# Kernel tuning notes

Measured on AMD Instinct MI355X. Metric: run time of the kernel, lower is better.

## Reference

```python
import jax, jax.numpy as jnp
import numpy as np

DIM = 96
D_STATE = 16
D_CONV = 3
D_INNER = 192   # int(DIM * 2.0)
DT_RANK = 6     # ceil(DIM / 16)
K = 4           # cross-scan directions
BATCH, H, W = 2, 56, 56


def setup_inputs() -> dict:
    key = jax.random.key(0)
    k = jax.random.split(key, 8)
    x = jax.random.normal(k[0], (BATCH, DIM, H, W), jnp.float32)
    W_in = jax.random.normal(k[1], (DIM, 2 * D_INNER), jnp.float32) / np.sqrt(DIM)
    W_conv = jax.random.normal(k[2], (D_INNER, 1, D_CONV, D_CONV), jnp.float32) / D_CONV
    b_conv = jnp.zeros((D_INNER,), jnp.float32)
    W_xproj = jax.random.normal(k[3], (K, D_INNER, DT_RANK + 2 * D_STATE), jnp.float32) / np.sqrt(D_INNER)
    W_dt = jax.random.normal(k[4], (K, DT_RANK, D_INNER), jnp.float32) / np.sqrt(DT_RANK)
    # dt bias init as in torch: dt ~ exp(U * (log 0.1 - log 0.001) + log 0.001), inv-softplus
    dt = jnp.exp(jax.random.uniform(k[5], (K, D_INNER), jnp.float32)
                 * (np.log(0.1) - np.log(0.001)) + np.log(0.001))
    dt = jnp.clip(dt, 1e-4, None)
    b_dt = dt + jnp.log(-jnp.expm1(-dt))
    A_logs = jnp.log(jnp.broadcast_to(jnp.arange(1, D_STATE + 1, dtype=jnp.float32),
                                      (K, D_INNER, D_STATE)))
    Ds = jnp.ones((K, D_INNER), jnp.float32)
    W_out = jax.random.normal(k[6], (D_INNER, DIM), jnp.float32) / np.sqrt(D_INNER)
    return dict(x=x, W_in=W_in, W_conv=W_conv, b_conv=b_conv, W_xproj=W_xproj,
                W_dt=W_dt, b_dt=b_dt, A_logs=A_logs, Ds=Ds, W_out=W_out)


def _ss2d(x, W_in, W_conv, b_conv, W_xproj, W_dt, b_dt, A_logs, Ds, W_out):
    Bsz, C, Hh, Ww = x.shape
    L = Hh * Ww
    # in_proj
    xf = x.transpose(0, 2, 3, 1).reshape(Bsz, L, C)        # (B, L, C)
    xz = xf @ W_in
    xp, z = jnp.split(xz, 2, axis=-1)                       # each (B, L, D)
    # depthwise conv + silu
    xi = xp.reshape(Bsz, Hh, Ww, -1).transpose(0, 3, 1, 2)  # (B, D, H, W)
    pad = D_CONV // 2
    xi = jax.lax.conv_general_dilated(
        xi, W_conv, (1, 1), ((pad, pad), (pad, pad)),
        feature_group_count=xi.shape[1],
        dimension_numbers=('NCHW', 'OIHW', 'NCHW')) + b_conv[None, :, None, None]
    xi = jax.nn.silu(xi)
    D = xi.shape[1]
    # cross-scan: 4 directions, each (B, L, D)
    x1 = xi.reshape(Bsz, D, L).transpose(0, 2, 1)
    x2 = xi[:, :, :, ::-1].reshape(Bsz, D, L).transpose(0, 2, 1)
    xt = xi.transpose(0, 1, 3, 2)                           # (B, D, W, H)
    x3 = xt.reshape(Bsz, D, L).transpose(0, 2, 1)
    x4 = xt[:, :, :, ::-1].reshape(Bsz, D, L).transpose(0, 2, 1)
    xs = jnp.stack([x1, x2, x3, x4])                        # (K, B, L, D)
    # per-direction projections, batched over K
    xdbl = jnp.einsum('kbld,kde->kble', xs, W_xproj)
    dr = xdbl[..., :DT_RANK]
    Bk = xdbl[..., DT_RANK:DT_RANK + D_STATE]               # (K, B, L, N)
    Ck = xdbl[..., DT_RANK + D_STATE:]                      # (K, B, L, N)
    delta = jax.nn.softplus(jnp.einsum('kblr,krd->kbld', dr, W_dt)
                            + b_dt[:, None, None, :])       # (K, B, L, D)
    A = -jnp.exp(A_logs)                                    # (K, D, N)

    def step(h, inp):
        x_i, d_i, B_i, C_i = inp  # (K,B,D), (K,B,D), (K,B,N), (K,B,N)
        dA = jnp.exp(d_i[..., None] * A[:, None])           # (K, B, D, N)
        h = dA * h + (d_i * x_i)[..., None] * B_i[:, :, None, :]
        y = jnp.einsum('kbdn,kbn->kbd', h, C_i)
        return h, y

    h0 = jnp.zeros((K, Bsz, D, D_STATE), xs.dtype)
    seq = (xs.transpose(2, 0, 1, 3), delta.transpose(2, 0, 1, 3),
           Bk.transpose(2, 0, 1, 3), Ck.transpose(2, 0, 1, 3))
    _, ys = jax.lax.scan(step, h0, seq)                     # (L, K, B, D)
    ys = ys.transpose(1, 2, 0, 3) + xs * Ds[:, None, None, :]  # (K, B, L, D)
    # cross-merge back to row-major (h w) order
    y1 = ys[0]
    y2 = ys[1].reshape(Bsz, Hh, Ww, D)[:, :, ::-1, :].reshape(Bsz, L, D)
    y3 = ys[2].reshape(Bsz, Ww, Hh, D).transpose(0, 2, 1, 3).reshape(Bsz, L, D)
    y4 = ys[3].reshape(Bsz, Ww, Hh, D)[:, :, ::-1, :].transpose(0, 2, 1, 3).reshape(Bsz, L, D)
    y = (y1 + y2 + y3 + y4) * jax.nn.silu(z)
    out = (y @ W_out).reshape(Bsz, Hh, Ww, C).transpose(0, 3, 1, 2)
    return out


def reference(x, W_in, W_conv, b_conv, W_xproj, W_dt, b_dt, A_logs, Ds, W_out):
    return _ss2d(x, W_in, W_conv, b_conv, W_xproj, W_dt, b_dt, A_logs, Ds, W_out)
```

## Files before the change

### kernel.cpp

```cpp
#include <hip/hip_runtime.h>
#include <math.h>

constexpr int BATCH  = 2;
constexpr int CDIM   = 96;
constexpr int HH     = 56;
constexpr int WW     = 56;
constexpr int LL     = HH * WW;
constexpr int DIN    = 192;
constexpr int NK     = 4;
constexpr int NST    = 16;
constexpr int RNK    = 6;
constexpr int EPROJ  = RNK + 2 * NST;
constexpr int SCH    = 64;
constexpr int NCH    = LL / SCH;
constexpr int CGRP   = DIN / 16;

constexpr int STDU = SCH + 2;
constexpr int STBC = SCH + 6;
constexpr int STY  = SCH + 4;
constexpr int STB1 = SCH + 4;

constexpr size_t SZ_PX   = (size_t)BATCH * LL * DIN;
constexpr size_t OFF_XP  = 0;
constexpr size_t OFF_Z   = OFF_XP + SZ_PX;
constexpr size_t OFF_XI  = OFF_Z  + SZ_PX;
constexpr size_t OFF_DR  = OFF_XI + SZ_PX;
constexpr size_t SZ_DR   = (size_t)NK * BATCH * LL * 8;
constexpr size_t OFF_B   = OFF_DR + SZ_DR;
constexpr size_t SZ_BC   = (size_t)NK * BATCH * LL * NST;
constexpr size_t OFF_C   = OFF_B + SZ_BC;
constexpr size_t OFF_YD  = OFF_C + SZ_BC;
constexpr size_t SZ_YD   = (size_t)NK * BATCH * LL * DIN;
constexpr size_t OFF_HE  = OFF_YD + SZ_YD;
constexpr size_t SZ_HS   = (size_t)NK * BATCH * NCH * DIN * NST;
constexpr size_t OFF_HI  = OFF_HE + SZ_HS;
constexpr size_t OFF_WT  = OFF_HI + SZ_HS;
constexpr size_t SZ_WT   = (size_t)NK * EPROJ * DIN;

__device__ __forceinline__ float silu(float v) {
    return v / (1.0f + __expf(-v));
}

__device__ __forceinline__ float softplus_f(float x) {
    return (x > 20.0f) ? x : __logf(1.0f + __expf(x));
}

__device__ __forceinline__ float row_reduce16(float p) {
    p += __int_as_float(__builtin_amdgcn_update_dpp(0, __float_as_int(p), 0x128, 0xf, 0xf, true));
    p += __int_as_float(__builtin_amdgcn_update_dpp(0, __float_as_int(p), 0x124, 0xf, 0xf, true));
    p += __int_as_float(__builtin_amdgcn_update_dpp(0, __float_as_int(p), 0x122, 0xf, 0xf, true));
    p += __int_as_float(__builtin_amdgcn_update_dpp(0, __float_as_int(p), 0x121, 0xf, 0xf, true));
    return p;
}

__device__ __forceinline__ int seq_to_lr(int k, int l) {
    int q = l / WW;
    int r = l - q * WW;
    if (k == 0) return l;
    if (k == 1) return q * WW + (WW - 1 - r);
    if (k == 2) return r * WW + q;
    return (WW - 1 - r) * WW + q;
}

__device__ __forceinline__ int spatial_to_seq(int k, int s) {
    int h = s / WW;
    int w = s - h * WW;
    if (k == 0) return s;
    if (k == 1) return h * WW + (WW - 1 - w);
    if (k == 2) return w * WW + h;
    return w * WW + (WW - 1 - h);
}

__device__ __forceinline__ size_t hs_idx(int c, int kb, int d, int n) {
    return ((size_t)(c * (NK * BATCH) + kb) * DIN + d) * NST + n;
}

__device__ __forceinline__ float4 delta4(
        float4 r03, float2 r45, const float4* wr, float4 bb4) {
    float4 raw = bb4;
    raw.x = fmaf(r03.x, wr[0].x, raw.x); raw.y = fmaf(r03.x, wr[0].y, raw.y);
    raw.z = fmaf(r03.x, wr[0].z, raw.z); raw.w = fmaf(r03.x, wr[0].w, raw.w);
    raw.x = fmaf(r03.y, wr[1].x, raw.x); raw.y = fmaf(r03.y, wr[1].y, raw.y);
    raw.z = fmaf(r03.y, wr[1].z, raw.z); raw.w = fmaf(r03.y, wr[1].w, raw.w);
    raw.x = fmaf(r03.z, wr[2].x, raw.x); raw.y = fmaf(r03.z, wr[2].y, raw.y);
    raw.z = fmaf(r03.z, wr[2].z, raw.z); raw.w = fmaf(r03.z, wr[2].w, raw.w);
    raw.x = fmaf(r03.w, wr[3].x, raw.x); raw.y = fmaf(r03.w, wr[3].y, raw.y);
    raw.z = fmaf(r03.w, wr[3].z, raw.z); raw.w = fmaf(r03.w, wr[3].w, raw.w);
    raw.x = fmaf(r45.x, wr[4].x, raw.x); raw.y = fmaf(r45.x, wr[4].y, raw.y);
    raw.z = fmaf(r45.x, wr[4].z, raw.z); raw.w = fmaf(r45.x, wr[4].w, raw.w);
    raw.x = fmaf(r45.y, wr[5].x, raw.x); raw.y = fmaf(r45.y, wr[5].y, raw.y);
    raw.z = fmaf(r45.y, wr[5].z, raw.z); raw.w = fmaf(r45.y, wr[5].w, raw.w);
    raw.x = softplus_f(raw.x); raw.y = softplus_f(raw.y);
    raw.z = softplus_f(raw.z); raw.w = softplus_f(raw.w);
    return raw;
}

constexpr int K1_PIX = 8;
__global__ __launch_bounds__(384) void k_inproj(
        const float* __restrict__ x, const float* __restrict__ W_in,
        const float* __restrict__ W_xproj,
        float* __restrict__ xp, float* __restrict__ z, float* __restrict__ Wt) {
    __shared__ float sxT[CDIM][K1_PIX];
    int gp0 = blockIdx.x * K1_PIX;
    int t   = threadIdx.x;
    int b   = gp0 / LL;
    int l0  = gp0 - b * LL;
    int gid = blockIdx.x * 384 + t;
    if (gid < NK * DIN * EPROJ) {
        int k = gid / (DIN * EPROJ);
        int r = gid % (DIN * EPROJ);
        int d = r / EPROJ;
        int e = r % EPROJ;
        Wt[((size_t)k * EPROJ + e) * DIN + d] = W_xproj[gid];
    }
    for (int i = t; i < CDIM * K1_PIX; i += 384) {
        int c = i >> 3, p = i & 7;
        sxT[c][p] = x[((size_t)(b * CDIM + c)) * LL + l0 + p];
    }
    __syncthreads();
    int e = t;
    float acc[K1_PIX];
#pragma unroll
    for (int p = 0; p < K1_PIX; p++) acc[p] = 0.0f;
    const float4* sx4 = (const float4*)sxT;
#pragma unroll 4
    for (int c = 0; c < CDIM; c++) {
        float w  = W_in[c * (2 * DIN) + e];
        float4 va = sx4[2 * c];
        float4 vb = sx4[2 * c + 1];
        acc[0] = fmaf(va.x, w, acc[0]); acc[1] = fmaf(va.y, w, acc[1]);
        acc[2] = fmaf(va.z, w, acc[2]); acc[3] = fmaf(va.w, w, acc[3]);
        acc[4] = fmaf(vb.x, w, acc[4]); acc[5] = fmaf(vb.y, w, acc[5]);
        acc[6] = fmaf(vb.z, w, acc[6]); acc[7] = fmaf(vb.w, w, acc[7]);
    }
    if (e < DIN) {
#pragma unroll
        for (int p = 0; p < K1_PIX; p++)
            xp[((size_t)(gp0 + p)) * DIN + e] = acc[p];
    } else {
        int e2 = e - DIN;
#pragma unroll
        for (int p = 0; p < K1_PIX; p++)
            z[((size_t)(gp0 + p)) * DIN + e2] = acc[p];
    }
}

__global__ __launch_bounds__(192) void k_conv(
        const float* __restrict__ xp, const float* __restrict__ Wc,
        const float* __restrict__ bc, float* __restrict__ xi) {
    int gp = blockIdx.x;
    int d  = threadIdx.x;
    int b  = gp / LL;
    int l  = gp - b * LL;
    int h  = l / WW;
    int w  = l - h * WW;
    float acc = bc[d];
#pragma unroll
    for (int dy = -1; dy <= 1; dy++) {
        int hh = h + dy;
        if (hh < 0 || hh >= HH) continue;
#pragma unroll
        for (int dx = -1; dx <= 1; dx++) {
            int ww = w + dx;
            if (ww < 0 || ww >= WW) continue;
            acc = fmaf(xp[((size_t)b * LL + hh * WW + ww) * DIN + d],
                       Wc[d * 9 + (dy + 1) * 3 + (dx + 1)], acc);
        }
    }
    xi[(size_t)gp * DIN + d] = silu(acc);
}

constexpr int K3_PIX = 32;
__global__ __launch_bounds__(256) void k_xproj(
        const float* __restrict__ xi, const float* __restrict__ Wt,
        float* __restrict__ drbuf, float* __restrict__ Bbuf,
        float* __restrict__ Cbuf) {
    __shared__ float4 v4[K3_PIX][49];
    __shared__ float4 sw4[EPROJ][49];
    int k   = blockIdx.y;
    int gp0 = blockIdx.x * K3_PIX;
    int b   = gp0 / LL;
    int l0  = gp0 - b * LL;
    int t   = threadIdx.x;
    const float4* xin4 = (const float4*)(xi + (size_t)gp0 * DIN);
    for (int i = t; i < K3_PIX * 48; i += 256)
        v4[i / 48][i % 48] = xin4[i];
    const float4* wt4 = (const float4*)(Wt + (size_t)k * EPROJ * DIN);
    for (int i = t; i < EPROJ * 48; i += 256)
        sw4[i / 48][i % 48] = wt4[i];
    __syncthreads();
    int p0 = t & 15;
    int eg = t >> 4;
    bool has3 = (eg < EPROJ - 32);
    float acc[2][3] = {{0.f, 0.f, 0.f}, {0.f, 0.f, 0.f}};
    for (int j = 0; j < 48; j++) {
        float4 w0 = sw4[eg][j];
        float4 w1 = sw4[eg + 16][j];
        float4 w2 = has3 ? sw4[eg + 32][j] : make_float4(0.f, 0.f, 0.f, 0.f);
#pragma unroll
        for (int q = 0; q < 2; q++) {
            float4 vv = v4[p0 + 16 * q][j];
            acc[q][0] = fmaf(vv.x, w0.x, acc[q][0]); acc[q][0] = fmaf(vv.y, w0.y, acc[q][0]);
            acc[q][0] = fmaf(vv.z, w0.z, acc[q][0]); acc[q][0] = fmaf(vv.w, w0.w, acc[q][0]);
            acc[q][1] = fmaf(vv.x, w1.x, acc[q][1]); acc[q][1] = fmaf(vv.y, w1.y, acc[q][1]);
            acc[q][1] = fmaf(vv.z, w1.z, acc[q][1]); acc[q][1] = fmaf(vv.w, w1.w, acc[q][1]);
            acc[q][2] = fmaf(vv.x, w2.x, acc[q][2]); acc[q][2] = fmaf(vv.y, w2.y, acc[q][2]);
            acc[q][2] = fmaf(vv.z, w2.z, acc[q][2]); acc[q][2] = fmaf(vv.w, w2.w, acc[q][2]);
        }
    }
#pragma unroll
    for (int q = 0; q < 2; q++) {
        int p  = p0 + 16 * q;
        int ls = spatial_to_seq(k, l0 + p);
        size_t kb  = (size_t)(k * BATCH + b);
        size_t b8  = (kb * LL + ls) * 8;
        size_t b16 = (kb * LL + ls) * NST;
        if (eg < RNK) drbuf[b8 + eg] = acc[q][0];
        else          Bbuf[b16 + eg - RNK] = acc[q][0];
        int e1 = eg + 16;
        if (e1 < RNK + NST) Bbuf[b16 + e1 - RNK] = acc[q][1];
        else                Cbuf[b16 + e1 - RNK - NST] = acc[q][1];
        if (has3) Cbuf[b16 + eg + 32 - RNK - NST] = acc[q][2];
    }
}

__global__ __launch_bounds__(256) void k_scanA(
        const float* __restrict__ xi, const float* __restrict__ drbuf,
        const float* __restrict__ Bbuf, const float* __restrict__ A_logs,
        const float* __restrict__ W_dt, const float* __restrict__ b_dt,
        float* __restrict__ Pbuf, float* __restrict__ hend) {
    __shared__ float2 sDU2[16][STDU];
    __shared__ float  sB1t[16][STB1];
    int c   = blockIdx.x;
    int blk = blockIdx.y;
    int k   = blk / (BATCH * CGRP);
    int rem = blk % (BATCH * CGRP);
    int b   = rem / CGRP;
    int cg  = rem % CGRP;
    int d0  = cg * 16;
    int t    = threadIdx.x;
    int lane = t & 63, wave = t >> 6;
    int grp  = lane >> 4, n = lane & 15;
    int ch   = wave * 4 + grp;
    int d    = d0 + ch;
    float A = -__expf(A_logs[((size_t)(k * DIN + d)) * NST + n]);
    size_t kb = (size_t)(k * BATCH + b);
    const float* drp = drbuf + kb * LL * 8;
    const float* bp  = Bbuf  + kb * LL * NST;
    const float* up  = xi    + (size_t)b * LL * DIN;
    int ss  = t >> 2;
    int cc0 = (t & 3) * 4;
    float4 wr[RNK];
#pragma unroll
    for (int r = 0; r < RNK; r++)
        wr[r] = *(const float4*)(W_dt + ((size_t)k * RNK + r) * DIN + d0 + cc0);
    float4 bb4 = *(const float4*)(b_dt + k * DIN + d0 + cc0);
    int l0 = c * SCH;
    {
        int l  = l0 + ss;
        int lr = seq_to_lr(k, l);
        float4 r03 = *(const float4*)(drp + (size_t)l * 8);
        float2 r45 = *(const float2*)(drp + (size_t)l * 8 + 4);
        float4 dlt = delta4(r03, r45, wr, bb4);
        float4 u4  = *(const float4*)(up + (size_t)lr * DIN + d0 + cc0);
        float4 B4  = *(const float4*)(bp + (size_t)l * NST + cc0);
        sDU2[cc0 + 0][ss] = make_float2(dlt.x, dlt.x * u4.x);
        sDU2[cc0 + 1][ss] = make_float2(dlt.y, dlt.y * u4.y);
        sDU2[cc0 + 2][ss] = make_float2(dlt.z, dlt.z * u4.z);
        sDU2[cc0 + 3][ss] = make_float2(dlt.w, dlt.w * u4.w);
        sB1t[cc0 + 0][ss] = B4.x;
        sB1t[cc0 + 1][ss] = B4.y;
        sB1t[cc0 + 2][ss] = B4.z;
        sB1t[cc0 + 3][ss] = B4.w;
    }
    __syncthreads();
    float h = 0.0f, P = 1.0f;
#pragma unroll 2
    for (int s4 = 0; s4 < SCH; s4 += 4) {
        float4 duA = *(const float4*)&sDU2[ch][s4];
        float4 duB = *(const float4*)&sDU2[ch][s4 + 2];
        float4 bq  = *(const float4*)&sB1t[n][s4];
        float dA;
        dA = __expf(duA.x * A); h = fmaf(dA, h, duA.y * bq.x); P *= dA;
        dA = __expf(duA.z * A); h = fmaf(dA, h, duA.w * bq.y); P *= dA;
        dA = __expf(duB.x * A); h = fmaf(dA, h, duB.y * bq.z); P *= dA;
        dA = __expf(duB.z * A); h = fmaf(dA, h, duB.w * bq.w); P *= dA;
    }
    size_t idx = hs_idx(c, (int)kb, d, n);
    Pbuf[idx] = P;
    hend[idx] = h;
}

__global__ __launch_bounds__(256) void k_scanB(
        const float* __restrict__ Pbuf, const float* __restrict__ hend,
        float* __restrict__ hin) {
    int tid = blockIdx.x * 256 + threadIdx.x;
    int kb  = tid / (DIN * NST);
    int dn  = tid % (DIN * NST);
    float h = 0.0f;
    for (int c = 0; c < NCH; c++) {
        size_t idx = ((size_t)(c * (NK * BATCH) + kb)) * (DIN * NST) + dn;
        hin[idx] = h;
        h = fmaf(Pbuf[idx], h, hend[idx]);
    }
}

__global__ __launch_bounds__(256) void k_scanC(
        const float* __restrict__ xi, const float* __restrict__ drbuf,
        const float* __restrict__ Bbuf, const float* __restrict__ Cbuf,
        const float* __restrict__ A_logs, const float* __restrict__ W_dt,
        const float* __restrict__ b_dt, const float* __restrict__ hin,
        float* __restrict__ ydir) {
    __shared__ float2 sDU2[16][STDU];
    __shared__ float2 sBC2[16][STBC];
    __shared__ float  sY[16][STY];
    int c   = blockIdx.x;
    int blk = blockIdx.y;
    int k   = blk / (BATCH * CGRP);
    int rem = blk % (BATCH * CGRP);
    int b   = rem / CGRP;
    int cg  = rem % CGRP;
    int d0  = cg * 16;
    int t    = threadIdx.x;
    int lane = t & 63, wave = t >> 6;
    int grp  = lane >> 4, n = lane & 15;
    int ch   = wave * 4 + grp;
    int d    = d0 + ch;
    float A = -__expf(A_logs[((size_t)(k * DIN + d)) * NST + n]);
    size_t kb = (size_t)(k * BATCH + b);
    const float* drp = drbuf + kb * LL * 8;
    const float* bp  = Bbuf  + kb * LL * NST;
    const float* cp  = Cbuf  + kb * LL * NST;
    const float* up  = xi    + (size_t)b * LL * DIN;
    float*       yp  = ydir  + kb * LL * DIN;
    int ss  = t >> 2;
    int cc0 = (t & 3) * 4;
    float4 wr[RNK];
#pragma unroll
    for (int r = 0; r < RNK; r++)
        wr[r] = *(const float4*)(W_dt + ((size_t)k * RNK + r) * DIN + d0 + cc0);
    float4 bb4 = *(const float4*)(b_dt + k * DIN + d0 + cc0);
    int l0 = c * SCH;
    {
        int l  = l0 + ss;
        int lr = seq_to_lr(k, l);
        float4 r03 = *(const float4*)(drp + (size_t)l * 8);
        float2 r45 = *(const float2*)(drp + (size_t)l * 8 + 4);
        float4 dlt = delta4(r03, r45, wr, bb4);
        float4 u4  = *(const float4*)(up + (size_t)lr * DIN + d0 + cc0);
        float4 B4  = *(const float4*)(bp + (size_t)l * NST + cc0);
        float4 C4  = *(const float4*)(cp + (size_t)l * NST + cc0);
        sDU2[cc0 + 0][ss] = make_float2(dlt.x, dlt.x * u4.x);
        sDU2[cc0 + 1][ss] = make_float2(dlt.y, dlt.y * u4.y);
        sDU2[cc0 + 2][ss] = make_float2(dlt.z, dlt.z * u4.z);
        sDU2[cc0 + 3][ss] = make_float2(dlt.w, dlt.w * u4.w);
        sBC2[cc0 + 0][ss] = make_float2(B4.x, C4.x);
        sBC2[cc0 + 1][ss] = make_float2(B4.y, C4.y);
        sBC2[cc0 + 2][ss] = make_float2(B4.z, C4.z);
        sBC2[cc0 + 3][ss] = make_float2(B4.w, C4.w);
    }
    float h = hin[hs_idx(c, (int)kb, d, n)];
    __syncthreads();
#pragma unroll 2
    for (int s4 = 0; s4 < SCH; s4 += 4) {
        float4 duA = *(const float4*)&sDU2[ch][s4];
        float4 duB = *(const float4*)&sDU2[ch][s4 + 2];
        float4 bcA = *(const float4*)&sBC2[n][s4];
        float4 bcB = *(const float4*)&sBC2[n][s4 + 2];
        float dA, y0, y1, y2, y3;
        dA = __expf(duA.x * A); h = fmaf(dA, h, duA.y * bcA.x); y0 = row_reduce16(h * bcA.y);
        dA = __expf(duA.z * A); h = fmaf(dA, h, duA.w * bcA.z); y1 = row_reduce16(h * bcA.w);
        dA = __expf(duB.x * A); h = fmaf(dA, h, duB.y * bcB.x); y2 = row_reduce16(h * bcB.y);
        dA = __expf(duB.z * A); h = fmaf(dA, h, duB.w * bcB.z); y3 = row_reduce16(h * bcB.w);
        if (n == 0) *(float4*)&sY[ch][s4] = make_float4(y0, y1, y2, y3);
    }
    __syncthreads();
    for (int i = t; i < SCH * 16; i += 256) {
        int s = i >> 4, cc = i & 15;
        int lr = seq_to_lr(k, l0 + s);
        yp[(size_t)lr * DIN + d0 + cc] = sY[cc][s];
    }
}

constexpr int K5_PIX = 8;
__global__ __launch_bounds__(192) void k_out(
        const float* __restrict__ ydir, const float* __restrict__ xi,
        const float* __restrict__ zbuf, const float* __restrict__ Ds,
        const float* __restrict__ W_out, float* __restrict__ out) {
    __shared__ float g[DIN][12];
    __shared__ float so[CDIM][9];
    int gp0 = blockIdx.x * K5_PIX;
    int b   = gp0 / LL;
    int l0  = gp0 - b * LL;
    int t   = threadIdx.x;
    for (int i = t; i < K5_PIX * DIN; i += 192) {
        int p = i / DIN, dd = i % DIN;
        size_t off = (size_t)(gp0 + p) * DIN + dd;
        float y = ydir[off] + ydir[SZ_PX + off]
                + ydir[2 * SZ_PX + off] + ydir[3 * SZ_PX + off];
        float dsum = Ds[dd] + Ds[DIN + dd] + Ds[2 * DIN + dd] + Ds[3 * DIN + dd];
        y = fmaf(xi[off], dsum, y);
        g[dd][p] = y * silu(zbuf[off]);
    }
    __syncthreads();
    int f    = t % CDIM;
    int half = t / CDIM;
    float acc[4] = {0.f, 0.f, 0.f, 0.f};
#pragma unroll 4
    for (int dd = 0; dd < DIN; dd++) {
        float wv = W_out[dd * CDIM + f];
        float4 gv = *(const float4*)&g[dd][half * 4];
        acc[0] = fmaf(gv.x, wv, acc[0]);
        acc[1] = fmaf(gv.y, wv, acc[1]);
        acc[2] = fmaf(gv.z, wv, acc[2]);
        acc[3] = fmaf(gv.w, wv, acc[3]);
    }
#pragma unroll
    for (int p = 0; p < 4; p++) so[f][half * 4 + p] = acc[p];
    __syncthreads();
    for (int i = t; i < CDIM * K5_PIX; i += 192) {
        int f2 = i / K5_PIX, p2 = i % K5_PIX;
        out[((size_t)(b * CDIM + f2)) * LL + l0 + p2] = so[f2][p2];
    }
}

extern "C" void kernel_launch(void* const* d_in, const int* in_sizes, int n_in,
                              void* d_out, int out_size, void* d_ws, size_t ws_size,
                              hipStream_t stream) {
    const float* x       = (const float*)d_in[0];
    const float* W_in    = (const float*)d_in[1];
    const float* W_conv  = (const float*)d_in[2];
    const float* b_conv  = (const float*)d_in[3];
    const float* W_xproj = (const float*)d_in[4];
    const float* W_dt    = (const float*)d_in[5];
    const float* b_dt    = (const float*)d_in[6];
    const float* A_logs  = (const float*)d_in[7];
    const float* Ds      = (const float*)d_in[8];
    const float* W_out   = (const float*)d_in[9];
    float* out = (float*)d_out;
    float* ws  = (float*)d_ws;

    float* xp    = ws + OFF_XP;
    float* z     = ws + OFF_Z;
    float* xi    = ws + OFF_XI;
    float* drbuf = ws + OFF_DR;
    float* Bbuf  = ws + OFF_B;
    float* Cbuf  = ws + OFF_C;
    float* ydir  = ws + OFF_YD;
    float* hend  = ws + OFF_HE;
    float* hin   = ws + OFF_HI;
    float* Wt    = ws + OFF_WT;
    float* Pbuf  = xp;

    k_inproj<<<(BATCH * LL) / K1_PIX, 384, 0, stream>>>(x, W_in, W_xproj, xp, z, Wt);
    k_conv<<<BATCH * LL, DIN, 0, stream>>>(xp, W_conv, b_conv, xi);
    dim3 g3((BATCH * LL) / K3_PIX, NK);
    k_xproj<<<g3, 256, 0, stream>>>(xi, Wt, drbuf, Bbuf, Cbuf);
    dim3 gs(NCH, NK * BATCH * CGRP);
    k_scanA<<<gs, 256, 0, stream>>>(xi, drbuf, Bbuf, A_logs, W_dt, b_dt, Pbuf, hend);
    k_scanB<<<(NK * BATCH * DIN * NST) / 256, 256, 0, stream>>>(Pbuf, hend, hin);
    k_scanC<<<gs, 256, 0, stream>>>(xi, drbuf, Bbuf, Cbuf, A_logs, W_dt, b_dt, hin, ydir);
    k_out<<<(BATCH * LL) / K5_PIX, 192, 0, stream>>>(ydir, xi, z, Ds, W_out, out);
}
```

Baseline: 212.5 us.

## Fuse chunk-prefix scan into scanC and read xproj weights from global

Removes the separate k_scanB kernel. Each scanC block now recomputes its own incoming chunk state by walking Pbuf/hend over all earlier chunks, which drops one launch and the hin buffer. The cost is redundant serial work that grows with the chunk index, up to 48 dependent loads per thread for late chunks. Separately, k_xproj stops staging the projection weights in shared memory and reads them straight from global (cached) memory with an unroll of 4, cutting LDS use and a staging loop.

```diff
diff --git a/kernel.cpp b/kernel.cpp
--- a/kernel.cpp
+++ b/kernel.cpp
@@ -33,8 +33,7 @@
 constexpr size_t SZ_YD   = (size_t)NK * BATCH * LL * DIN;
 constexpr size_t OFF_HE  = OFF_YD + SZ_YD;
 constexpr size_t SZ_HS   = (size_t)NK * BATCH * NCH * DIN * NST;
-constexpr size_t OFF_HI  = OFF_HE + SZ_HS;
-constexpr size_t OFF_WT  = OFF_HI + SZ_HS;
+constexpr size_t OFF_WT  = OFF_HE + SZ_HS;
 constexpr size_t SZ_WT   = (size_t)NK * EPROJ * DIN;
 
 __device__ __forceinline__ float silu(float v) {
@@ -176,7 +175,6 @@
         float* __restrict__ drbuf, float* __restrict__ Bbuf,
         float* __restrict__ Cbuf) {
     __shared__ float4 v4[K3_PIX][49];
-    __shared__ float4 sw4[EPROJ][49];
     int k   = blockIdx.y;
     int gp0 = blockIdx.x * K3_PIX;
     int b   = gp0 / LL;
@@ -186,17 +184,16 @@
     for (int i = t; i < K3_PIX * 48; i += 256)
         v4[i / 48][i % 48] = xin4[i];
     const float4* wt4 = (const float4*)(Wt + (size_t)k * EPROJ * DIN);
-    for (int i = t; i < EPROJ * 48; i += 256)
-        sw4[i / 48][i % 48] = wt4[i];
     __syncthreads();
     int p0 = t & 15;
     int eg = t >> 4;
     bool has3 = (eg < EPROJ - 32);
     float acc[2][3] = {{0.f, 0.f, 0.f}, {0.f, 0.f, 0.f}};
+#pragma unroll 4
     for (int j = 0; j < 48; j++) {
-        float4 w0 = sw4[eg][j];
-        float4 w1 = sw4[eg + 16][j];
-        float4 w2 = has3 ? sw4[eg + 32][j] : make_float4(0.f, 0.f, 0.f, 0.f);
+        float4 w0 = wt4[eg * 48 + j];
+        float4 w1 = wt4[(eg + 16) * 48 + j];
+        float4 w2 = has3 ? wt4[(eg + 32) * 48 + j] : make_float4(0.f, 0.f, 0.f, 0.f);
 #pragma unroll
         for (int q = 0; q < 2; q++) {
             float4 vv = v4[p0 + 16 * q][j];
@@ -291,25 +288,12 @@
     hend[idx] = h;
 }
 
-__global__ __launch_bounds__(256) void k_scanB(
-        const float* __restrict__ Pbuf, const float* __restrict__ hend,
-        float* __restrict__ hin) {
-    int tid = blockIdx.x * 256 + threadIdx.x;
-    int kb  = tid / (DIN * NST);
-    int dn  = tid % (DIN * NST);
-    float h = 0.0f;
-    for (int c = 0; c < NCH; c++) {
-        size_t idx = ((size_t)(c * (NK * BATCH) + kb)) * (DIN * NST) + dn;
-        hin[idx] = h;
-        h = fmaf(Pbuf[idx], h, hend[idx]);
-    }
-}
-
 __global__ __launch_bounds__(256) void k_scanC(
         const float* __restrict__ xi, const float* __restrict__ drbuf,
         const float* __restrict__ Bbuf, const float* __restrict__ Cbuf,
         const float* __restrict__ A_logs, const float* __restrict__ W_dt,
-        const float* __restrict__ b_dt, const float* __restrict__ hin,
+        const float* __restrict__ b_dt,
+        const float* __restrict__ Pbuf, const float* __restrict__ hend,
         float* __restrict__ ydir) {
     __shared__ float2 sDU2[16][STDU];
     __shared__ float2 sBC2[16][STBC];
@@ -333,6 +317,11 @@
     const float* cp  = Cbuf  + kb * LL * NST;
     const float* up  = xi    + (size_t)b * LL * DIN;
     float*       yp  = ydir  + kb * LL * DIN;
+    float hin = 0.0f;
+    for (int j = 0; j < c; j++) {
+        size_t jx = hs_idx(j, (int)kb, d, n);
+        hin = fmaf(Pbuf[jx], hin, hend[jx]);
+    }
     int ss  = t >> 2;
     int cc0 = (t & 3) * 4;
     float4 wr[RNK];
@@ -359,8 +348,8 @@
         sBC2[cc0 + 2][ss] = make_float2(B4.z, C4.z);
         sBC2[cc0 + 3][ss] = make_float2(B4.w, C4.w);
     }
-    float h = hin[hs_idx(c, (int)kb, d, n)];
-    __syncthreads();
+    __syncthreads();
+    float h = hin;
 #pragma unroll 2
     for (int s4 = 0; s4 < SCH; s4 += 4) {
         float4 duA = *(const float4*)&sDU2[ch][s4];
@@ -448,7 +437,6 @@
     float* Cbuf  = ws + OFF_C;
     float* ydir  = ws + OFF_YD;
     float* hend  = ws + OFF_HE;
-    float* hin   = ws + OFF_HI;
     float* Wt    = ws + OFF_WT;
     float* Pbuf  = xp;
 
@@ -458,7 +446,6 @@
     k_xproj<<<g3, 256, 0, stream>>>(xi, Wt, drbuf, Bbuf, Cbuf);
     dim3 gs(NCH, NK * BATCH * CGRP);
     k_scanA<<<gs, 256, 0, stream>>>(xi, drbuf, Bbuf, A_logs, W_dt, b_dt, Pbuf, hend);
-    k_scanB<<<(NK * BATCH * DIN * NST) / 256, 256, 0, stream>>>(Pbuf, hend, hin);
-    k_scanC<<<gs, 256, 0, stream>>>(xi, drbuf, Bbuf, Cbuf, A_logs, W_dt, b_dt, hin, ydir);
+    k_scanC<<<gs, 256, 0, stream>>>(xi, drbuf, Bbuf, Cbuf, A_logs, W_dt, b_dt, Pbuf, hend, ydir);
     k_out<<<(BATCH * LL) / K5_PIX, 192, 0, stream>>>(ydir, xi, z, Ds, W_out, out);
 }
```

Result: no change. 215.3 us (+1.3%).
